# Kernel tuning notes

Hardware: AMD Instinct MI355X
Metric: run time of the kernel (lower is better)

The kernel has to match this reference:

```python
import jax, jax.numpy as jnp
import numpy as np


def _diag_perm(h, w):
    # Matches torch loop: offsets -(h-1)..w-1, within offset ordered by row i.
    ii, jj = np.meshgrid(np.arange(h), np.arange(w), indexing='ij')
    idx = np.lexsort((ii.ravel(), (jj - ii).ravel())).astype(np.int32)
    inv = np.argsort(idx).astype(np.int32)
    return jnp.asarray(idx), jnp.asarray(inv)


def _mamba(tok, ln_g, ln_b, Win, conv_w, conv_b, Wx, Wdt, bdt, A_log, Dp, Wout):
    # tok: (B, L, C). MambaLayer = LayerNorm + standard Mamba block.
    di, dc = conv_w.shape
    ds = A_log.shape[-1]
    dtr = Wdt.shape[-1]
    mu = tok.mean(-1, keepdims=True)
    var = ((tok - mu) ** 2).mean(-1, keepdims=True)
    t = (tok - mu) * jax.lax.rsqrt(var + 1e-5) * ln_g + ln_b
    xz = jnp.einsum('blc,ec->ble', t, Win)          # (B,L,2*di)
    xh, z = jnp.split(xz, 2, axis=-1)
    # causal depthwise conv over sequence
    xc = jnp.transpose(xh, (0, 2, 1))               # (B,di,L)
    xc = jax.lax.conv_general_dilated(
        xc, conv_w[:, None, :], (1,), [(dc - 1, 0)],
        dimension_numbers=('NCH', 'OIH', 'NCH'), feature_group_count=di)
    u = jax.nn.silu(jnp.transpose(xc, (0, 2, 1)) + conv_b)  # (B,L,di)
    proj = jnp.einsum('bld,ed->ble', u, Wx)
    dt_r, Bm, Cm = jnp.split(proj, [dtr, dtr + ds], axis=-1)
    dt = jax.nn.softplus(jnp.einsum('blr,dr->bld', dt_r, Wdt) + bdt)  # (B,L,di)
    A = -jnp.exp(A_log)                              # (di,ds)

    def step(h, inp):
        dt_t, B_t, C_t, u_t = inp                    # (B,di) (B,ds) (B,ds) (B,di)
        dA = jnp.exp(dt_t[..., None] * A)            # (B,di,ds)
        h = dA * h + dt_t[..., None] * B_t[:, None, :] * u_t[..., None]
        y = jnp.einsum('bds,bs->bd', h, C_t)
        return h, y

    h0 = jnp.zeros((u.shape[0], di, ds), u.dtype)
    _, ys = jax.lax.scan(step, h0, (jnp.moveaxis(dt, 1, 0), jnp.moveaxis(Bm, 1, 0),
                                    jnp.moveaxis(Cm, 1, 0), jnp.moveaxis(u, 1, 0)))
    y = jnp.moveaxis(ys, 0, 1) + u * Dp              # (B,L,di)
    y = y * jax.nn.silu(z)
    return jnp.einsum('bld,cd->blc', y, Wout)


def _forward(x, ln_g, ln_b, Win, conv_w, conv_b, Wx, Wdt, bdt, A_log, Dp, Wout):
    b, c, h, w = x.shape
    idx, inv = _diag_perm(h, w)

    def mam(d, tok):
        return _mamba(tok, ln_g[d], ln_b[d], Win[d], conv_w[d], conv_b[d],
                      Wx[d], Wdt[d], bdt[d], A_log[d], Dp[d], Wout[d])

    row_tok = x.reshape(b, c, h * w).transpose(0, 2, 1)
    row_feat = mam(0, row_tok).transpose(0, 2, 1).reshape(b, c, h, w)
    col_tok = x.transpose(0, 1, 3, 2).reshape(b, c, w * h).transpose(0, 2, 1)
    col_feat = mam(1, col_tok).transpose(0, 2, 1).reshape(b, c, w, h).transpose(0, 1, 3, 2)
    diag_feat = mam(2, row_tok[:, idx, :])[:, inv, :].transpose(0, 2, 1).reshape(b, c, h, w)
    xf = x[:, :, :, ::-1]
    anti_tok = xf.reshape(b, c, h * w).transpose(0, 2, 1)[:, idx, :]
    anti_feat = mam(3, anti_tok)[:, inv, :].transpose(0, 2, 1).reshape(b, c, h, w)[:, :, :, ::-1]
    gate = jax.nn.sigmoid((row_feat + col_feat + diag_feat + anti_feat) / 4.0)
    return x * gate


def setup_inputs() -> dict:
    key = jax.random.key(0)
    ks = jax.random.split(key, 8)
    B, C, H, W = 4, 96, 48, 48
    DI, DS, DC, DTR = 192, 16, 4, 6
    s = 0.05
    return {
        'x': jax.random.normal(ks[0], (B, C, H, W), jnp.float32),
        'ln_g': jnp.ones((4, C), jnp.float32),
        'ln_b': jnp.zeros((4, C), jnp.float32),
        'Win': jax.random.normal(ks[1], (4, 2 * DI, C), jnp.float32) * s,
        'conv_w': jax.random.normal(ks[2], (4, DI, DC), jnp.float32) * s,
        'conv_b': jnp.zeros((4, DI), jnp.float32),
        'Wx': jax.random.normal(ks[3], (4, DTR + 2 * DS, DI), jnp.float32) * s,
        'Wdt': jax.random.normal(ks[4], (4, DI, DTR), jnp.float32) * s,
        'bdt': jax.random.normal(ks[5], (4, DI), jnp.float32) * s,
        'A_log': jnp.log(jnp.broadcast_to(jnp.arange(1, DS + 1, dtype=jnp.float32), (4, DI, DS))),
        'Dp': jnp.ones((4, DI), jnp.float32),
        'Wout': jax.random.normal(ks[6], (4, C, DI), jnp.float32) * s,
    }


def reference(x, ln_g, ln_b, Win, conv_w, conv_b, Wx, Wdt, bdt, A_log, Dp, Wout):
    return _forward(x, ln_g, ln_b, Win, conv_w, conv_b, Wx, Wdt, bdt, A_log, Dp, Wout)
```

## Files before the change

### kernel.cpp

```cpp
#include <hip/hip_runtime.h>
#include <math.h>

#define LSEQ 2304
#define LC 32
#define NCH 72

typedef unsigned short u16;
typedef unsigned int u32;
typedef __attribute__((ext_vector_type(8))) short bf16x8;
typedef __attribute__((ext_vector_type(4))) float f32x4;

__device__ __forceinline__ float sigmoidf_(float v){ return 1.f/(1.f+__expf(-v)); }
__device__ __forceinline__ u16 f2b(float f){
  union{float f; u32 u;} v; v.f = f;
  u32 r = v.u + 0x7fffu + ((v.u >> 16) & 1u);
  return (u16)(r >> 16);
}
__device__ __forceinline__ float b2f(u16 h){
  union{u32 u; float f;} v; v.u = ((u32)h) << 16; return v.f;
}
__device__ __forceinline__ u16 f2h(float f){
  _Float16 h = (_Float16)f;
  union{_Float16 h; u16 u;} v; v.h = h; return v.u;
}
__device__ __forceinline__ float h2f(u16 u){
  union{u16 u; _Float16 h;} v; v.u = u; return (float)v.h;
}
__device__ __forceinline__ uint2 pack4(float a, float b, float c, float d){
  uint2 o;
  o.x = (u32)f2b(a) | ((u32)f2b(b) << 16);
  o.y = (u32)f2b(c) | ((u32)f2b(d) << 16);
  return o;
}
__device__ __forceinline__ float softplus_(float v){
  return fmaxf(v, 0.f) + __logf(1.f + __expf(-fabsf(v)));
}

__global__ __launch_bounds__(256) void prep_fold(const float* __restrict__ Win, const float* __restrict__ ln_g,
                          const float* __restrict__ ln_b, const float* __restrict__ A_log,
                          const float* __restrict__ Wout, const float* __restrict__ Wx,
                          const float* __restrict__ Wdt, const float* __restrict__ bdt,
                          const float* __restrict__ x,
                          u16* __restrict__ WinMF, float* __restrict__ b2,
                          float* __restrict__ Aneg2, u16* __restrict__ WoutMF,
                          u16* __restrict__ Wcomb, float* __restrict__ bcomb,
                          int* __restrict__ g, int* __restrict__ invg, int* __restrict__ flag,
                          u16* __restrict__ n){
  __shared__ float red[512];
  if (blockIdx.x >= 768){
    int tid = threadIdx.x;
    int s = tid & 63, q = tid >> 6;
    int T = (blockIdx.x - 768) * 64 + s;
    int b = T / 2304, p = T % 2304;
    const float* xp = x + (size_t)b * 96 * 2304 + p;
    float vals[24];
    float sum = 0.f, ss = 0.f;
    #pragma unroll
    for (int k = 0; k < 24; ++k){
      float v = xp[(size_t)(q*24 + k) * 2304];
      vals[k] = v; sum += v; ss += v*v;
    }
    red[q*64 + s] = sum;
    red[256 + q*64 + s] = ss;
    __syncthreads();
    float S = red[s] + red[64+s] + red[128+s] + red[192+s];
    float Q = red[256+s] + red[320+s] + red[384+s] + red[448+s];
    float mu = S * (1.f/96.f);
    float var = Q * (1.f/96.f) - mu*mu;
    float rs = rsqrtf(var + 1e-5f);
    u32 w[12];
    #pragma unroll
    for (int k = 0; k < 12; ++k){
      float v0 = (vals[2*k]   - mu) * rs;
      float v1 = (vals[2*k+1] - mu) * rs;
      w[k] = (u32)f2b(v0) | ((u32)f2b(v1) << 16);
    }
    uint4* np_ = (uint4*)(n + (size_t)T * 96 + q*24);
    np_[0] = make_uint4(w[0], w[1], w[2],  w[3]);
    np_[1] = make_uint4(w[4], w[5], w[6],  w[7]);
    np_[2] = make_uint4(w[8], w[9], w[10], w[11]);
    return;
  }
  int i = blockIdx.x * 256 + threadIdx.x;
  if (i < LSEQ){
    int l = i;
    g[l] = l;
    g[LSEQ + l] = (l % 48) * 48 + l / 48;
    invg[l] = l;
    invg[LSEQ + l] = (l % 48) * 48 + l / 48;
    int p = i;
    int ii = p / 48, jj = p % 48, dd = jj - ii;
    int off = (dd <= 0) ? (47 + dd) * (48 + dd) / 2
                        : 1176 + 48 * (dd - 1) - dd * (dd - 1) / 2;
    int l2 = off + min(ii, jj);
    g[2 * LSEQ + l2] = p;
    g[3 * LSEQ + l2] = ii * 48 + 47 - jj;
    invg[2 * LSEQ + p] = l2;
    invg[3 * LSEQ + ii * 48 + 47 - jj] = l2;
  }
  if (i < 4*192*16){
    float a = -expf(A_log[i]);
    Aneg2[i] = a * 1.44269504f;
    int s = i & 15;
    float a0 = -expf(A_log[i - s]);
    if (fabsf(a - (float)(s + 1) * a0) > 1e-5f * fabsf(a) + 1e-30f)
      atomicOr(flag, 1);
  }
  if (i < 4*384*96){
    int d = i / 36864, r = i % 36864, c = r % 96;
    WinMF[i] = f2b(Win[i] * ln_g[d*96 + c]);
  }
  if (i < 4*96*192) WoutMF[i] = f2b(Wout[i]);
  if (i < 4*224*192){
    int d = i / 43008, r = i % 43008, e = r / 192, c = r % 192;
    float w;
    if (e < 192){
      const float* wdt = &Wdt[(size_t)(d*192 + e) * 6];
      w = 0.f;
      #pragma unroll
      for (int r6 = 0; r6 < 6; ++r6) w += wdt[r6] * Wx[(size_t)(d*38 + r6) * 192 + c];
    } else if (e < 208){
      w = Wx[(size_t)(d*38 + 6 + (e - 192)) * 192 + c];
    } else {
      w = Wx[(size_t)(d*38 + 22 + (e - 208)) * 192 + c];
    }
    Wcomb[i] = f2b(w);
  }
  if (i < 4*224){
    int d = i / 224, e = i % 224;
    bcomb[i] = (e < 192) ? bdt[d*192 + e] : 0.f;
  }
  if (i < 4*384){
    int d = i / 384;
    const float* wr = &Win[(size_t)i * 96];
    const float* lb = &ln_b[d * 96];
    float s = 0.f;
    for (int c = 0; c < 96; ++c) s += wr[c] * lb[c];
    b2[i] = s;
  }
}

__global__ __launch_bounds__(256) void kproj(const u16* __restrict__ nbf,
    const u16* __restrict__ WinMF, const float* __restrict__ b2,
    const int* __restrict__ invg, u16* __restrict__ xz, u16* __restrict__ sz){
  int d = blockIdx.y;
  int wv = threadIdx.x >> 6, lane = threadIdx.x & 63;
  int lr = lane & 15, lg = lane >> 4;
  int r0 = blockIdx.x * 64 + wv * 16;
  int row = r0 + lr;
  int b = row / 2304, p = row % 2304;
  const u16* Ap = nbf + (size_t)row * 96 + lg * 8;
  bf16x8 tk0 = *(const bf16x8*)(Ap);
  bf16x8 tk1 = *(const bf16x8*)(Ap + 32);
  bf16x8 tk2 = *(const bf16x8*)(Ap + 64);
  const u16* Wb = WinMF + (size_t)d * 36864 + (size_t)lr * 96 + lg * 8;
  const float* b2d = b2 + d * 384;
  u16* outx = xz + ((size_t)d * 9216 + row) * 192;
  int lseq = invg[d * LSEQ + p];
  u16* outz = sz + ((size_t)(d*4 + b) * LSEQ + lseq) * 192;
  for (int grp = 0; grp < 3; ++grp){
    f32x4 acc[8];
    #pragma unroll
    for (int t = 0; t < 8; ++t)
      acc[t] = *(const f32x4*)&b2d[(grp*8 + t)*16 + lg*4];
    #pragma unroll
    for (int t = 0; t < 8; ++t){
      const u16* wp = Wb + (size_t)(grp*8 + t) * 1536;
      acc[t] = __builtin_amdgcn_mfma_f32_16x16x32_bf16(*(const bf16x8*)(wp     ), tk0, acc[t], 0, 0, 0);
      acc[t] = __builtin_amdgcn_mfma_f32_16x16x32_bf16(*(const bf16x8*)(wp + 32), tk1, acc[t], 0, 0, 0);
      acc[t] = __builtin_amdgcn_mfma_f32_16x16x32_bf16(*(const bf16x8*)(wp + 64), tk2, acc[t], 0, 0, 0);
    }
    #pragma unroll
    for (int t = 0; t < 8; ++t){
      int te = grp*8 + t;
      if (te < 12){
        uint2 o = pack4(acc[t][0], acc[t][1], acc[t][2], acc[t][3]);
        *(uint2*)&outx[te*16 + lg*4] = o;
      } else {
        float z0 = acc[t][0], z1 = acc[t][1], z2 = acc[t][2], z3 = acc[t][3];
        z0 *= sigmoidf_(z0); z1 *= sigmoidf_(z1); z2 *= sigmoidf_(z2); z3 *= sigmoidf_(z3);
        *(uint2*)&outz[(te-12)*16 + lg*4] = pack4(z0, z1, z2, z3);
      }
    }
  }
}

__global__ __launch_bounds__(256) void kconvBM(const u16* __restrict__ xz, const int* __restrict__ g,
    const float* __restrict__ conv_w, const float* __restrict__ conv_b,
    const u16* __restrict__ Wcomb, const float* __restrict__ bcomb,
    u16* __restrict__ u, u16* __restrict__ dtb, float* __restrict__ Bm, float* __restrict__ Cm){
  __shared__ u16 xh[67*200];
  int d = blockIdx.z, b = blockIdx.y, l0 = blockIdx.x * 64;
  int tid = threadIdx.x;
  const int* gd = g + d * LSEQ;
  const u16* xzd = xz + (size_t)d * 9216 * 192 + (size_t)b * LSEQ * 192;
  for (int i = tid; i < 67*24; i += 256){
    int lt = i / 24, j = i % 24;
    int gl = l0 - 3 + lt;
    uint4 v = make_uint4(0u, 0u, 0u, 0u);
    if (gl >= 0){
      int p = gd[gl];
      v = *(const uint4*)(xzd + (size_t)p * 192 + j * 8);
    }
    *(uint4*)&xh[lt*200 + j*8] = v;
  }
  __syncthreads();
  uint2 ures[12];
  #pragma unroll
  for (int it = 0; it < 12; ++it){
    int i = tid + it*256;
    int lt = i / 48, j = (i % 48) * 4;
    float a0 = conv_b[d*192 + j + 0];
    float a1 = conv_b[d*192 + j + 1];
    float a2 = conv_b[d*192 + j + 2];
    float a3 = conv_b[d*192 + j + 3];
    const float4 w0 = *(const float4*)&conv_w[(size_t)(d*192 + j + 0) * 4];
    const float4 w1 = *(const float4*)&conv_w[(size_t)(d*192 + j + 1) * 4];
    const float4 w2 = *(const float4*)&conv_w[(size_t)(d*192 + j + 2) * 4];
    const float4 w3 = *(const float4*)&conv_w[(size_t)(d*192 + j + 3) * 4];
    const float* w0p = (const float*)&w0;
    const float* w1p = (const float*)&w1;
    const float* w2p = (const float*)&w2;
    const float* w3p = (const float*)&w3;
    #pragma unroll
    for (int kk = 0; kk < 4; ++kk){
      uint2 xv = *(const uint2*)&xh[(lt + kk)*200 + j];
      a0 += w0p[kk] * b2f((u16)(xv.x & 0xffff));
      a1 += w1p[kk] * b2f((u16)(xv.x >> 16));
      a2 += w2p[kk] * b2f((u16)(xv.y & 0xffff));
      a3 += w3p[kk] * b2f((u16)(xv.y >> 16));
    }
    a0 *= sigmoidf_(a0); a1 *= sigmoidf_(a1); a2 *= sigmoidf_(a2); a3 *= sigmoidf_(a3);
    ures[it] = pack4(a0, a1, a2, a3);
  }
  __syncthreads();
  size_t obase = ((size_t)(d*4 + b) * LSEQ + l0) * 192;
  #pragma unroll
  for (int it = 0; it < 12; ++it){
    int i = tid + it*256;
    int lt = i / 48, j = (i % 48) * 4;
    *(uint2*)&xh[lt*200 + j] = ures[it];
    *(uint2*)(u + obase + (size_t)lt * 192 + j) = ures[it];
  }
  __syncthreads();
  int wv = tid >> 6, lane = tid & 63;
  int lr = lane & 15, lg = lane >> 4;
  const u16* urow = &xh[(wv*16 + lr)*200 + lg*8];
  bf16x8 tk[6];
  #pragma unroll
  for (int kc = 0; kc < 6; ++kc) tk[kc] = *(const bf16x8*)(urow + kc*32);
  const u16* Wb = Wcomb + (size_t)d * 224 * 192 + (size_t)lr * 192 + lg * 8;
  bf16x8 bw[2][6];
  #pragma unroll
  for (int kc = 0; kc < 6; ++kc) bw[0][kc] = *(const bf16x8*)(Wb + kc*32);
  size_t tokrow = (size_t)(d*4 + b) * LSEQ + l0 + wv*16 + lr;
  for (int t = 0; t < 14; ++t){
    int cur = t & 1;
    if (t < 13){
      const u16* wp = Wb + (size_t)(t + 1) * 3072;
      #pragma unroll
      for (int kc = 0; kc < 6; ++kc) bw[cur^1][kc] = *(const bf16x8*)(wp + kc*32);
    }
    f32x4 a = (f32x4){0.f, 0.f, 0.f, 0.f};
    #pragma unroll
    for (int kc = 0; kc < 6; ++kc)
      a = __builtin_amdgcn_mfma_f32_16x16x32_bf16(bw[cur][kc], tk[kc], a, 0, 0, 0);
    if (t < 12){
      f32x4 bb = *(const f32x4*)&bcomb[d*224 + t*16 + lg*4];
      float s0 = softplus_(a[0] + bb[0]);
      float s1 = softplus_(a[1] + bb[1]);
      float s2 = softplus_(a[2] + bb[2]);
      float s3 = softplus_(a[3] + bb[3]);
      uint2 o;
      o.x = (u32)f2h(s0) | ((u32)f2h(s1) << 16);
      o.y = (u32)f2h(s2) | ((u32)f2h(s3) << 16);
      *(uint2*)&dtb[tokrow * 192 + t*16 + lg*4] = o;
    } else if (t == 12){
      *(float4*)&Bm[tokrow * 16 + lg*4] = make_float4(a[0], a[1], a[2], a[3]);
    } else {
      *(float4*)&Cm[tokrow * 16 + lg*4] = make_float4(a[0], a[1], a[2], a[3]);
    }
  }
}

__global__ __launch_bounds__(192) void kernC1(const u16* __restrict__ dtb, const u16* __restrict__ u,
    const float* __restrict__ Bm, const float* __restrict__ Cm,
    const float* __restrict__ Aneg2, const float* __restrict__ Dp, const int* __restrict__ flag,
    u16* __restrict__ hfin, float* __restrict__ Send, u32* __restrict__ yS){
  __shared__ float Bsh[LC*16];
  __shared__ float Csh[LC*16];
  __shared__ u16 dtsh[LC*192];
  __shared__ u16 ush2[LC*192];
  int ch = blockIdx.x, b = blockIdx.y, d = blockIdx.z;
  int seq = d*4 + b;
  int di = threadIdx.x;
  size_t tb = (size_t)seq * LSEQ + ch * LC;
  const float* bp = Bm + tb * 16;
  const float* cp = Cm + tb * 16;
  for (int i = di; i < LC*16; i += 192){ Bsh[i] = bp[i]; Csh[i] = cp[i]; }
  {
    const uint4* dt4 = (const uint4*)(dtb + tb * 192);
    const uint4* u4  = (const uint4*)(u   + tb * 192);
    #pragma unroll
    for (int i = di; i < LC*24; i += 192){
      *(uint4*)&dtsh[i*8] = dt4[i];
      *(uint4*)&ush2[i*8] = u4[i];
    }
  }
  u32* ySp = yS + tb * 192;
  float Dpv = Dp[d*192 + di];
  float h[16];
  #pragma unroll
  for (int s = 0; s < 16; ++s) h[s] = 0.f;
  float Sacc = 0.f;
  __syncthreads();
  if (*flag == 0){
    float A2_0 = Aneg2[(d*192 + di) * 16];
    for (int j = 0; j < LC; ++j){
      float dtv = h2f(dtsh[j*192 + di]);
      float uv  = b2f(ush2[j*192 + di]);
      float Bs[16], Cs[16];
      {
        const float4* b4 = (const float4*)&Bsh[j * 16];
        const float4* c4 = (const float4*)&Csh[j * 16];
        #pragma unroll
        for (int q = 0; q < 4; ++q){
          float4 v = b4[q]; Bs[q*4]=v.x; Bs[q*4+1]=v.y; Bs[q*4+2]=v.z; Bs[q*4+3]=v.w;
          float4 w = c4[q]; Cs[q*4]=w.x; Cs[q*4+1]=w.y; Cs[q*4+2]=w.z; Cs[q*4+3]=w.w;
        }
      }
      float dtu = dtv * uv;
      float e1 = __builtin_amdgcn_exp2f(dtv * A2_0);
      float e2 = e1*e1, e4 = e2*e2, e8 = e4*e4;
      float p[8];
      p[0]=e1; p[1]=e2; p[2]=e1*e2; p[3]=e4; p[4]=e1*e4; p[5]=e2*e4; p[6]=p[2]*e4; p[7]=e8;
      float yv = uv * Dpv;
      #pragma unroll
      for (int s = 0; s < 8; ++s){
        h[s] = p[s]*h[s] + dtu*Bs[s];
        yv += h[s]*Cs[s];
        float q = p[s]*e8;
        h[s+8] = q*h[s+8] + dtu*Bs[s+8];
        yv += h[s+8]*Cs[s+8];
      }
      Sacc += dtv;
      ySp[j*192 + di] = (u32)f2h(yv) | ((u32)f2h(Sacc) << 16);
    }
  } else {
    float A2[16];
    {
      const float4* ap = (const float4*)&Aneg2[(d*192 + di) * 16];
      #pragma unroll
      for (int q = 0; q < 4; ++q){ float4 a4 = ap[q]; A2[q*4]=a4.x; A2[q*4+1]=a4.y; A2[q*4+2]=a4.z; A2[q*4+3]=a4.w; }
    }
    for (int j = 0; j < LC; ++j){
      float dtv = h2f(dtsh[j*192 + di]);
      float uv  = b2f(ush2[j*192 + di]);
      float Bs[16], Cs[16];
      {
        const float4* b4 = (const float4*)&Bsh[j * 16];
        const float4* c4 = (const float4*)&Csh[j * 16];
        #pragma unroll
        for (int q = 0; q < 4; ++q){
          float4 v = b4[q]; Bs[q*4]=v.x; Bs[q*4+1]=v.y; Bs[q*4+2]=v.z; Bs[q*4+3]=v.w;
          float4 w = c4[q]; Cs[q*4]=w.x; Cs[q*4+1]=w.y; Cs[q*4+2]=w.z; Cs[q*4+3]=w.w;
        }
      }
      float dtu = dtv * uv;
      float yv = uv * Dpv;
      #pragma unroll
      for (int s = 0; s < 16; ++s){
        h[s] = __builtin_amdgcn_exp2f(dtv * A2[s]) * h[s] + dtu * Bs[s];
        yv += h[s] * Cs[s];
      }
      Sacc += dtv;
      ySp[j*192 + di] = (u32)f2h(yv) | ((u32)f2h(Sacc) << 16);
    }
  }
  u16* hf = &hfin[((size_t)seq * NCH + ch) * 3072 + di * 16];
  uint4 o0, o1;
  o0.x = (u32)f2b(h[0])  | ((u32)f2b(h[1])  << 16);
  o0.y = (u32)f2b(h[2])  | ((u32)f2b(h[3])  << 16);
  o0.z = (u32)f2b(h[4])  | ((u32)f2b(h[5])  << 16);
  o0.w = (u32)f2b(h[6])  | ((u32)f2b(h[7])  << 16);
  o1.x = (u32)f2b(h[8])  | ((u32)f2b(h[9])  << 16);
  o1.y = (u32)f2b(h[10]) | ((u32)f2b(h[11]) << 16);
  o1.z = (u32)f2b(h[12]) | ((u32)f2b(h[13]) << 16);
  o1.w = (u32)f2b(h[14]) | ((u32)f2b(h[15]) << 16);
  *(uint4*)hf = o0;
  *(uint4*)(hf + 8) = o1;
  Send[((size_t)seq * NCH + ch) * 192 + di] = Sacc;
}

__global__ __launch_bounds__(256) void kernC2(const u16* __restrict__ hfin, const float* __restrict__ Send,
    const float* __restrict__ Aneg2, u16* __restrict__ hin){
  int t = blockIdx.x * 256 + threadIdx.x;
  int seq = t / 3072, q = t % 3072;
  int di = q >> 4, s = q & 15;
  int d = seq >> 2;
  float A2 = Aneg2[(d*192 + di)*16 + s];
  float hr = 0.f;
  const u16* hf = hfin + (size_t)seq * NCH * 3072 + q;
  u16* hi = hin + (size_t)seq * NCH * 3072 + q;
  const float* Se = Send + (size_t)seq * NCH * 192 + di;
  for (int ch = 0; ch < NCH; ch += 8){
    float Se8[8]; u16 hf8[8];
    #pragma unroll
    for (int k = 0; k < 8; ++k){
      Se8[k] = Se[(size_t)(ch+k) * 192];
      hf8[k] = hf[(size_t)(ch+k) * 3072];
    }
    #pragma unroll
    for (int k = 0; k < 8; ++k){
      hi[(size_t)(ch+k) * 3072] = f2b(hr);
      hr = b2f(hf8[k]) + __builtin_amdgcn_exp2f(A2 * Se8[k]) * hr;
    }
  }
}

__global__ __launch_bounds__(384) void kscan2out(const u32* __restrict__ yS,
    const float* __restrict__ Cm,
    const float* __restrict__ Aneg2, const int* __restrict__ flag, const u16* __restrict__ hin,
    const u16* __restrict__ sz,
    const u16* __restrict__ WoutMF, const int* __restrict__ g,
    u16* __restrict__ feat){
  __shared__ float Csh[64*16];
  __shared__ u16 vsh[64][200];
  int b = blockIdx.y, d = blockIdx.z;
  int seq = d*4 + b;
  int l0 = blockIdx.x * 64;
  int tid = threadIdx.x;
  int gc = tid / 192, di = tid % 192;
  int ch = blockIdx.x * 2 + gc;
  {
    const float* cp = Cm + ((size_t)seq * LSEQ + l0) * 16;
    for (int i = tid; i < 64*16; i += 384) Csh[i] = cp[i];
  }
  float hs[16];
  {
    const uint4* hi4 = (const uint4*)&hin[((size_t)seq * NCH + ch) * 3072 + di * 16];
    uint4 v0 = hi4[0], v1 = hi4[1];
    hs[0]=b2f((u16)(v0.x&0xffff)); hs[1]=b2f((u16)(v0.x>>16));
    hs[2]=b2f((u16)(v0.y&0xffff)); hs[3]=b2f((u16)(v0.y>>16));
    hs[4]=b2f((u16)(v0.z&0xffff)); hs[5]=b2f((u16)(v0.z>>16));
    hs[6]=b2f((u16)(v0.w&0xffff)); hs[7]=b2f((u16)(v0.w>>16));
    hs[8]=b2f((u16)(v1.x&0xffff)); hs[9]=b2f((u16)(v1.x>>16));
    hs[10]=b2f((u16)(v1.y&0xffff)); hs[11]=b2f((u16)(v1.y>>16));
    hs[12]=b2f((u16)(v1.z&0xffff)); hs[13]=b2f((u16)(v1.z>>16));
    hs[14]=b2f((u16)(v1.w&0xffff)); hs[15]=b2f((u16)(v1.w>>16));
  }
  size_t tb = (size_t)seq * LSEQ + ch * LC;
  const u32* ySp = yS + tb * 192;
  const u16* szp = sz  + tb * 192;
  __syncthreads();
  if (*flag == 0){
    float A2_0 = Aneg2[(d*192 + di) * 16];
    #pragma unroll
    for (int jb = 0; jb < 4; ++jb){
      u32 ys8[8]; u16 zz8[8];
      #pragma unroll
      for (int k = 0; k < 8; ++k){
        int j = jb*8 + k;
        ys8[k] = ySp[j*192 + di];
        zz8[k] = szp[j*192 + di];
      }
      #pragma unroll
      for (int k = 0; k < 8; ++k){
        int j = jb*8 + k;
        float yv = h2f((u16)(ys8[k] & 0xffff));
        float Sc = h2f((u16)(ys8[k] >> 16));
        float Cs[16];
        {
          const float4* c4 = (const float4*)&Csh[(gc*32 + j) * 16];
          #pragma unroll
          for (int q = 0; q < 4; ++q){ float4 w = c4[q]; Cs[q*4]=w.x; Cs[q*4+1]=w.y; Cs[q*4+2]=w.z; Cs[q*4+3]=w.w; }
        }
        float e1 = __builtin_amdgcn_exp2f(Sc * A2_0);
        float e2 = e1*e1, e4 = e2*e2, e8 = e4*e4;
        float p[8];
        p[0]=e1; p[1]=e2; p[2]=e1*e2; p[3]=e4; p[4]=e1*e4; p[5]=e2*e4; p[6]=p[2]*e4; p[7]=e8;
        float corr = 0.f;
        #pragma unroll
        for (int s = 0; s < 8; ++s){
          corr += p[s]    * hs[s]   * Cs[s];
          corr += p[s]*e8 * hs[s+8] * Cs[s+8];
        }
        float szv = b2f(zz8[k]);
        vsh[gc*32 + j][di] = f2b((yv + corr) * szv);
      }
    }
  } else {
    float A2[16];
    {
      const float4* ap = (const float4*)&Aneg2[(d*192 + di) * 16];
      #pragma unroll
      for (int q = 0; q < 4; ++q){ float4 a4 = ap[q]; A2[q*4]=a4.x; A2[q*4+1]=a4.y; A2[q*4+2]=a4.z; A2[q*4+3]=a4.w; }
    }
    #pragma unroll
    for (int jb = 0; jb < 4; ++jb){
      u32 ys8[8]; u16 zz8[8];
      #pragma unroll
      for (int k = 0; k < 8; ++k){
        int j = jb*8 + k;
        ys8[k] = ySp[j*192 + di];
        zz8[k] = szp[j*192 + di];
      }
      #pragma unroll
      for (int k = 0; k < 8; ++k){
        int j = jb*8 + k;
        float yv = h2f((u16)(ys8[k] & 0xffff));
        float Sc = h2f((u16)(ys8[k] >> 16));
        float Cs[16];
        {
          const float4* c4 = (const float4*)&Csh[(gc*32 + j) * 16];
          #pragma unroll
          for (int q = 0; q < 4; ++q){ float4 w = c4[q]; Cs[q*4]=w.x; Cs[q*4+1]=w.y; Cs[q*4+2]=w.z; Cs[q*4+3]=w.w; }
        }
        float corr = 0.f;
        #pragma unroll
        for (int s = 0; s < 16; ++s)
          corr += __builtin_amdgcn_exp2f(Sc * A2[s]) * hs[s] * Cs[s];
        float szv = b2f(zz8[k]);
        vsh[gc*32 + j][di] = f2b((yv + corr) * szv);
      }
    }
  }
  __syncthreads();
  if (tid < 256){
    int wv = tid >> 6, lane = tid & 63;
    int lr = lane & 15, lg = lane >> 4;
    bf16x8 tk[6];
    #pragma unroll
    for (int kc = 0; kc < 6; ++kc)
      tk[kc] = *(const bf16x8*)&vsh[wv*16 + lr][kc*32 + lg*8];
    const u16* Wb = WoutMF + (size_t)d * 18432 + (size_t)lr * 192 + lg * 8;
    f32x4 acc[6];
    #pragma unroll
    for (int t = 0; t < 6; ++t) acc[t] = (f32x4){0.f, 0.f, 0.f, 0.f};
    #pragma unroll
    for (int t = 0; t < 6; ++t){
      const u16* wp = Wb + (size_t)t * 3072;
      #pragma unroll
      for (int kc = 0; kc < 6; ++kc)
        acc[t] = __builtin_amdgcn_mfma_f32_16x16x32_bf16(*(const bf16x8*)(wp + kc*32), tk[kc], acc[t], 0, 0, 0);
    }
    u16* fd = feat + (size_t)seq * LSEQ * 96;
    int p = g[d*LSEQ + l0 + wv*16 + lr];
    #pragma unroll
    for (int t = 0; t < 6; ++t){
      uint2 o = pack4(acc[t][0], acc[t][1], acc[t][2], acc[t][3]);
      *(uint2*)&fd[(size_t)p * 96 + t*16 + lg*4] = o;
    }
  }
}

__global__ __launch_bounds__(256) void kernE(const float* __restrict__ x, const u16* __restrict__ feat,
    float* __restrict__ out){
  __shared__ float acc[64 * 97];
  int p0 = blockIdx.x * 64, b = blockIdx.y;
  int tid = threadIdx.x;
  const size_t DS_ = (size_t)4 * LSEQ * 96;
  size_t base = ((size_t)b * LSEQ + p0) * 96;
  for (int i = tid; i < 3072; i += 256){
    int pp = i / 48, c2 = (i % 48) * 2;
    size_t o = base + (size_t)pp * 96 + c2;
    u32 v0 = *(const u32*)(feat + o);
    u32 v1 = *(const u32*)(feat + DS_ + o);
    u32 v2 = *(const u32*)(feat + 2*DS_ + o);
    u32 v3 = *(const u32*)(feat + 3*DS_ + o);
    float s0 = b2f((u16)(v0 & 0xffff)) + b2f((u16)(v1 & 0xffff)) + b2f((u16)(v2 & 0xffff)) + b2f((u16)(v3 & 0xffff));
    float s1 = b2f((u16)(v0 >> 16)) + b2f((u16)(v1 >> 16)) + b2f((u16)(v2 >> 16)) + b2f((u16)(v3 >> 16));
    acc[pp*97 + c2] = s0;
    acc[pp*97 + c2 + 1] = s1;
  }
  __syncthreads();
  for (int i = tid; i < 6144; i += 256){
    int c = i / 64, pp = i % 64;
    size_t o = ((size_t)b * 96 + c) * LSEQ + p0 + pp;
    out[o] = x[o] * sigmoidf_(acc[pp*97 + c] * 0.25f);
  }
}

extern "C" void kernel_launch(void* const* d_in, const int* in_sizes, int n_in,
                              void* d_out, int out_size, void* d_ws, size_t ws_size,
                              hipStream_t stream) {
  const float* x      = (const float*)d_in[0];
  const float* ln_g   = (const float*)d_in[1];
  const float* ln_b   = (const float*)d_in[2];
  const float* Win    = (const float*)d_in[3];
  const float* conv_w = (const float*)d_in[4];
  const float* conv_b = (const float*)d_in[5];
  const float* Wx     = (const float*)d_in[6];
  const float* Wdt    = (const float*)d_in[7];
  const float* bdt    = (const float*)d_in[8];
  const float* A_log  = (const float*)d_in[9];
  const float* Dp     = (const float*)d_in[10];
  const float* Wout   = (const float*)d_in[11];

  char* W = (char*)d_ws;
  char* W0 = W;
  auto alloc = [&](size_t bytes) -> char* {
    char* p = W; W += (bytes + 255) & ~(size_t)255; return p;
  };
  int*   g      = (int*)  alloc((size_t)4 * LSEQ * 4);
  int*   invg   = (int*)  alloc((size_t)4 * LSEQ * 4);
  int*   flag   = (int*)  alloc(256);
  float* Aneg2  = (float*)alloc((size_t)4 * 192 * 16 * 4);
  float* b2     = (float*)alloc((size_t)4 * 384 * 4);
  u16*   WinMF  = (u16*)  alloc((size_t)4 * 384 * 96 * 2);
  u16*   WoutMF = (u16*)  alloc((size_t)4 * 96 * 192 * 2);
  u16*   Wcomb  = (u16*)  alloc((size_t)4 * 224 * 192 * 2);
  float* bcomb  = (float*)alloc((size_t)4 * 224 * 4);
  u16*   nbf    = (u16*)  alloc((size_t)9216 * 96 * 2);
  u16*   xz     = (u16*)  alloc((size_t)4 * 9216 * 192 * 2);
  u16*   ubf    = (u16*)  alloc((size_t)16 * LSEQ * 192 * 2);
  u16*   szbf   = (u16*)  alloc((size_t)16 * LSEQ * 192 * 2);
  u16*   dtb    = (u16*)  alloc((size_t)16 * LSEQ * 192 * 2);
  float* Bm     = (float*)alloc((size_t)16 * LSEQ * 16 * 4);
  float* Cm     = (float*)alloc((size_t)16 * LSEQ * 16 * 4);
  u32*   ySbuf  = (u32*)  alloc((size_t)16 * LSEQ * 192 * 4);
  float* Send   = (float*)alloc((size_t)16 * NCH * 192 * 4);
  u16*   hfin   = (u16*)  alloc((size_t)16 * NCH * 3072 * 2);
  u16*   hin    = (u16*)  alloc((size_t)16 * NCH * 3072 * 2);
  u16*   feat   = (u16*)  alloc((size_t)16 * LSEQ * 96 * 2);
  if ((size_t)(W - W0) > ws_size) return;

  hipMemsetAsync(flag, 0, sizeof(int), stream);
  prep_fold<<<912, 256, 0, stream>>>(Win, ln_g, ln_b, A_log, Wout, Wx, Wdt, bdt, x,
                                     WinMF, b2, Aneg2, WoutMF, Wcomb, bcomb, g, invg, flag, nbf);
  kproj<<<dim3(144, 4), 256, 0, stream>>>(nbf, WinMF, b2, invg, xz, szbf);
  kconvBM<<<dim3(36, 4, 4), 256, 0, stream>>>(xz, g, conv_w, conv_b, Wcomb, bcomb,
                                              ubf, dtb, Bm, Cm);
  kernC1<<<dim3(NCH, 4, 4), 192, 0, stream>>>(dtb, ubf, Bm, Cm, Aneg2, Dp, flag, hfin, Send, ySbuf);
  kernC2<<<192, 256, 0, stream>>>(hfin, Send, Aneg2, hin);
  kscan2out<<<dim3(36, 4, 4), 384, 0, stream>>>(ySbuf, Cm, Aneg2, flag, hin, szbf,
                                                WoutMF, g, feat);
  kernE<<<dim3(36, 4), 256, 0, stream>>>(x, feat, (float*)d_out);
}
```

Measured before the change: 173.9 us.

## Split fused conv+BM kernel into separate conv and projection kernels

Splits the fused causal-conv plus dt/B/C projection kernel into two launches. One kernel computes the depthwise conv and SiLU and writes u to global memory. A second kernel reloads u tiles into shared memory and runs the MFMA projection. This lowers per-kernel register and LDS pressure and may raise occupancy, but it adds a kernel launch and a global round-trip of u.

Result: slower. 179.6 us (+3.2%).

```diff
diff --git a/kernel.cpp b/kernel.cpp
--- a/kernel.cpp
+++ b/kernel.cpp
@@ -185,11 +185,10 @@
   }
 }
 
-__global__ __launch_bounds__(256) void kconvBM(const u16* __restrict__ xz, const int* __restrict__ g,
+__global__ __launch_bounds__(256) void kconv(const u16* __restrict__ xz, const int* __restrict__ g,
     const float* __restrict__ conv_w, const float* __restrict__ conv_b,
-    const u16* __restrict__ Wcomb, const float* __restrict__ bcomb,
-    u16* __restrict__ u, u16* __restrict__ dtb, float* __restrict__ Bm, float* __restrict__ Cm){
-  __shared__ u16 xh[67*200];
+    u16* __restrict__ u){
+  __shared__ u16 xh[67][200];
   int d = blockIdx.z, b = blockIdx.y, l0 = blockIdx.x * 64;
   int tid = threadIdx.x;
   const int* gd = g + d * LSEQ;
@@ -202,13 +201,11 @@
       int p = gd[gl];
       v = *(const uint4*)(xzd + (size_t)p * 192 + j * 8);
     }
-    *(uint4*)&xh[lt*200 + j*8] = v;
+    *(uint4*)&xh[lt][j*8] = v;
   }
   __syncthreads();
-  uint2 ures[12];
-  #pragma unroll
-  for (int it = 0; it < 12; ++it){
-    int i = tid + it*256;
+  size_t obase = ((size_t)(d*4 + b) * LSEQ + l0) * 192;
+  for (int i = tid; i < 64*48; i += 256){
     int lt = i / 48, j = (i % 48) * 4;
     float a0 = conv_b[d*192 + j + 0];
     float a1 = conv_b[d*192 + j + 1];
@@ -224,28 +221,33 @@
     const float* w3p = (const float*)&w3;
     #pragma unroll
     for (int kk = 0; kk < 4; ++kk){
-      uint2 xv = *(const uint2*)&xh[(lt + kk)*200 + j];
+      uint2 xv = *(const uint2*)&xh[lt + kk][j];
       a0 += w0p[kk] * b2f((u16)(xv.x & 0xffff));
       a1 += w1p[kk] * b2f((u16)(xv.x >> 16));
       a2 += w2p[kk] * b2f((u16)(xv.y & 0xffff));
       a3 += w3p[kk] * b2f((u16)(xv.y >> 16));
     }
     a0 *= sigmoidf_(a0); a1 *= sigmoidf_(a1); a2 *= sigmoidf_(a2); a3 *= sigmoidf_(a3);
-    ures[it] = pack4(a0, a1, a2, a3);
-  }
-  __syncthreads();
-  size_t obase = ((size_t)(d*4 + b) * LSEQ + l0) * 192;
-  #pragma unroll
-  for (int it = 0; it < 12; ++it){
-    int i = tid + it*256;
-    int lt = i / 48, j = (i % 48) * 4;
-    *(uint2*)&xh[lt*200 + j] = ures[it];
-    *(uint2*)(u + obase + (size_t)lt * 192 + j) = ures[it];
+    *(uint2*)(u + obase + (size_t)lt * 192 + j) = pack4(a0, a1, a2, a3);
+  }
+}
+
+__global__ __launch_bounds__(256) void kernBM(const u16* __restrict__ u,
+    const u16* __restrict__ Wcomb, const float* __restrict__ bcomb,
+    u16* __restrict__ dtb, float* __restrict__ Bm, float* __restrict__ Cm){
+  __shared__ u16 ush[64 * 200];
+  int d = blockIdx.y;
+  int tid = threadIdx.x;
+  int tile0 = blockIdx.x * 64;
+  const u16* ub = u + ((size_t)d * 4 * LSEQ + tile0) * 192;
+  for (int i = tid; i < 64*24; i += 256){
+    int row = i / 24, c8 = i % 24;
+    *(uint4*)&ush[row*200 + c8*8] = *(const uint4*)&ub[(size_t)row*192 + c8*8];
   }
   __syncthreads();
   int wv = tid >> 6, lane = tid & 63;
   int lr = lane & 15, lg = lane >> 4;
-  const u16* urow = &xh[(wv*16 + lr)*200 + lg*8];
+  const u16* urow = &ush[(wv*16 + lr)*200 + lg*8];
   bf16x8 tk[6];
   #pragma unroll
   for (int kc = 0; kc < 6; ++kc) tk[kc] = *(const bf16x8*)(urow + kc*32);
@@ -253,7 +255,7 @@
   bf16x8 bw[2][6];
   #pragma unroll
   for (int kc = 0; kc < 6; ++kc) bw[0][kc] = *(const bf16x8*)(Wb + kc*32);
-  size_t tokrow = (size_t)(d*4 + b) * LSEQ + l0 + wv*16 + lr;
+  size_t tokrow = (size_t)d * 4 * LSEQ + tile0 + wv*16 + lr;
   for (int t = 0; t < 14; ++t){
     int cur = t & 1;
     if (t < 13){
@@ -629,8 +631,8 @@
   prep_fold<<<912, 256, 0, stream>>>(Win, ln_g, ln_b, A_log, Wout, Wx, Wdt, bdt, x,
                                      WinMF, b2, Aneg2, WoutMF, Wcomb, bcomb, g, invg, flag, nbf);
   kproj<<<dim3(144, 4), 256, 0, stream>>>(nbf, WinMF, b2, invg, xz, szbf);
-  kconvBM<<<dim3(36, 4, 4), 256, 0, stream>>>(xz, g, conv_w, conv_b, Wcomb, bcomb,
-                                              ubf, dtb, Bm, Cm);
+  kconv<<<dim3(36, 4, 4), 256, 0, stream>>>(xz, g, conv_w, conv_b, ubf);
+  kernBM<<<dim3(144, 4), 256, 0, stream>>>(ubf, Wcomb, bcomb, dtb, Bm, Cm);
   kernC1<<<dim3(NCH, 4, 4), 192, 0, stream>>>(dtb, ubf, Bm, Cm, Aneg2, Dp, flag, hfin, Send, ySbuf);
   kernC2<<<192, 256, 0, stream>>>(hfin, Send, Aneg2, hin);
   kscan2out<<<dim3(36, 4, 4), 384, 0, stream>>>(ySbuf, Cm, Aneg2, flag, hin, szbf,
```
